# Kernel tuning notes

Measured on AMD Instinct MI355X. Metric: run time of the kernel, lower is better.

Reference implementation:

```python
import jax, jax.numpy as jnp
import numpy as np

B, T, D, H = 4096, 48, 64, 128
IMPUTE_WEIGHT = 0.3


def setup_inputs() -> dict:
    key = jax.random.key(0)
    ks = jax.random.split(key, 16)
    values = jax.random.normal(ks[0], (B, T, D), dtype=jnp.float32)
    masks = (jax.random.uniform(ks[1], (B, T, D)) < 0.7).astype(jnp.float32)
    deltas = jax.random.uniform(ks[2], (B, T, D), dtype=jnp.float32)
    s = 0.05
    return {
        "values": values, "masks": masks, "deltas": deltas,
        # TemporalDecay h (non-diag): Linear(D -> H)
        "W_td_h": jax.random.normal(ks[3], (H, D), dtype=jnp.float32) * s,
        "b_td_h": jax.random.normal(ks[4], (H,), dtype=jnp.float32) * s,
        # TemporalDecay x (diag): W is D x D but only diagonal used
        "W_td_x": jax.random.normal(ks[5], (D, D), dtype=jnp.float32) * s,
        "b_td_x": jax.random.normal(ks[6], (D,), dtype=jnp.float32) * s,
        # hist_reg: Linear(H -> D)
        "W_hist": jax.random.normal(ks[7], (D, H), dtype=jnp.float32) * s,
        "b_hist": jax.random.normal(ks[8], (D,), dtype=jnp.float32) * s,
        # feat_reg: D x D with zeroed diagonal mask
        "W_feat": jax.random.normal(ks[9], (D, D), dtype=jnp.float32) * s,
        "b_feat": jax.random.normal(ks[10], (D,), dtype=jnp.float32) * s,
        # weight_combine: Linear(2D -> D)
        "W_comb": jax.random.normal(ks[11], (D, 2 * D), dtype=jnp.float32) * s,
        "b_comb": jax.random.normal(ks[12], (D,), dtype=jnp.float32) * s,
        # LSTMCell(2D -> H), torch gate order i,f,g,o
        "W_ih": jax.random.normal(ks[13], (4 * H, 2 * D), dtype=jnp.float32) * s,
        "W_hh": jax.random.normal(ks[14], (4 * H, H), dtype=jnp.float32) * s,
        "b_ih": jnp.zeros((4 * H,), dtype=jnp.float32),
        "b_hh": jnp.zeros((4 * H,), dtype=jnp.float32),
    }


def reference(values, masks, deltas, W_td_h, b_td_h, W_td_x, b_td_x,
              W_hist, b_hist, W_feat, b_feat, W_comb, b_comb,
              W_ih, W_hh, b_ih, b_hh):
    Bn, Tn, Dn = values.shape
    Hn = W_hh.shape[1]
    w_td_x_diag = jnp.diagonal(W_td_x)                      # diag mask -> elementwise
    W_feat_m = W_feat * (1.0 - jnp.eye(Dn, dtype=W_feat.dtype))  # zero diagonal

    def step(carry, xs):
        h, c, x_loss = carry
        x, m, d = xs                                        # each [B, D]
        gamma_h = jnp.exp(-jax.nn.relu(d @ W_td_h.T + b_td_h))   # [B, H]
        gamma_x = jnp.exp(-jax.nn.relu(d * w_td_x_diag + b_td_x))  # [B, D]
        h = h * gamma_h
        x_h = h @ W_hist.T + b_hist
        denom = jnp.sum(m) + 1e-5
        x_loss = x_loss + jnp.sum(jnp.abs(x - x_h) * m) / denom
        x_c = m * x + (1.0 - m) * x_h
        z_h = x_c @ W_feat_m.T + b_feat
        x_loss = x_loss + jnp.sum(jnp.abs(x - z_h) * m) / denom
        alpha = jnp.concatenate([gamma_x, m], axis=1) @ W_comb.T + b_comb
        c_h = alpha * z_h + (1.0 - alpha) * x_h
        x_loss = x_loss + jnp.sum(jnp.abs(x - c_h) * m) / denom
        c_c = m * x + (1.0 - m) * c_h
        inp = jnp.concatenate([c_c, m], axis=1)             # [B, 2D]
        gates = inp @ W_ih.T + b_ih + h @ W_hh.T + b_hh     # [B, 4H]
        i_g, f_g, g_g, o_g = jnp.split(gates, 4, axis=1)
        c = jax.nn.sigmoid(f_g) * c + jax.nn.sigmoid(i_g) * jnp.tanh(g_g)
        h = jax.nn.sigmoid(o_g) * jnp.tanh(c)
        return (h, c, x_loss), c_c

    h0 = jnp.zeros((Bn, Hn), dtype=values.dtype)
    c0 = jnp.zeros((Bn, Hn), dtype=values.dtype)
    xs = (jnp.swapaxes(values, 0, 1), jnp.swapaxes(masks, 0, 1), jnp.swapaxes(deltas, 0, 1))
    (_, _, x_loss), imps = jax.lax.scan(step, (h0, c0, jnp.float32(0.0)), xs)
    imputations = jnp.swapaxes(imps, 0, 1)                  # [B, T, D]
    loss = x_loss * IMPUTE_WEIGHT
    return loss, imputations
```

## Files before the change

### kernel.cpp

```cpp
#include <hip/hip_runtime.h>
#include <cmath>

#define Bb 4096
#define Tt 48
#define Dd 64
#define Hh 128
#define NB 16
#define NTHR 512

#define BAR_LDS() asm volatile("s_waitcnt lgkmcnt(0)\n\ts_barrier" ::: "memory")

typedef unsigned short ushort_t;
typedef __attribute__((ext_vector_type(8))) short short8;
typedef __attribute__((ext_vector_type(4))) float floatx4;

#define WS_DEN   0
#define WS_LOSS  48
#define WS_FRAGS 64
#define FR_F 0
#define FR_A 256
#define FR_B 272
#define FR_C 288
#define FR_E 296
#define N_FRAGS 312

__device__ __forceinline__ ushort_t f2bf(float x) {
  unsigned int u = __float_as_uint(x);
  u += 0x7fffu + ((u >> 16) & 1u);
  return (ushort_t)(u >> 16);
}
__device__ __forceinline__ float sigmoidf_(float x) { return 1.0f / (1.0f + __expf(-x)); }
__device__ __forceinline__ float tanhf_(float x) { return 2.0f / (1.0f + __expf(-2.0f * x)) - 1.0f; }

__global__ void prep_kernel(const float* __restrict__ W_td_h, const float* __restrict__ W_hist,
                            const float* __restrict__ W_feat, const float* __restrict__ W_comb,
                            const float* __restrict__ W_ih, const float* __restrict__ W_hh,
                            float* __restrict__ ws) {
  int f = blockIdx.x;
  int tid = threadIdx.x;
  if (f == 0 && tid < 64) ws[tid] = 0.0f;
  ushort_t* fb = (ushort_t*)(ws + WS_FRAGS);
  #pragma unroll
  for (int u = 0; u < 2; u++) {
    int e = tid * 2 + u;
    int l = e >> 3, j = e & 7;
    int n16 = l & 15;
    int kq = ((l >> 4) << 3) + j;
    float v;
    if (f < 256) {
      int w = f >> 5, g = (f >> 3) & 3, ks = f & 7;
      int n = g * 128 + w * 16 + n16;
      int k = ks * 32 + kq;
      v = (k < 128) ? W_ih[n * 128 + k] : W_hh[n * 128 + (k - 128)];
    } else if (f < 272) {
      int ff = f - 256, w = ff >> 1, ks = ff & 1;
      int n = w * 16 + n16;
      v = W_td_h[n * 64 + ks * 32 + kq];
    } else if (f < 288) {
      int ff = f - 272, w = ff >> 2, ks = ff & 3;
      int n = w * 16 + n16;
      v = W_hist[n * 128 + ks * 32 + kq];
    } else if (f < 296) {
      int ff = f - 288, w = ff >> 1, ks = ff & 1;
      int n = w * 16 + n16;
      int k = ks * 32 + kq;
      v = (n == k) ? 0.0f : W_feat[n * 64 + k];
    } else {
      int ff = f - 296, w = ff >> 2, ks = ff & 3;
      int n = w * 16 + n16;
      v = W_comb[n * 128 + ks * 32 + kq];
    }
    fb[f * 512 + e] = f2bf(v);
  }
}

__global__ void denom_kernel(const float* __restrict__ masks, float* __restrict__ ws) {
  int t = blockIdx.x >> 4;
  int chunk = blockIdx.x & 15;
  int base = chunk * 256;
  int tid = threadIdx.x;
  int j = tid & 63;
  int brow = tid >> 6;
  float s = 0.0f;
  for (int i = 0; i < 64; i++) {
    int b = base + i * 4 + brow;
    s += masks[((size_t)b * Tt + t) * Dd + j];
  }
  for (int off = 32; off > 0; off >>= 1) s += __shfl_down(s, off, 64);
  __shared__ float red[4];
  if ((tid & 63) == 0) red[tid >> 6] = s;
  __syncthreads();
  if (tid == 0) atomicAdd(&ws[WS_DEN + t], red[0] + red[1] + red[2] + red[3]);
}

__global__ __launch_bounds__(NTHR, 2)
void main_kernel(const float* __restrict__ values, const float* __restrict__ masks,
                 const float* __restrict__ deltas, const float* __restrict__ W_td_x,
                 const float* __restrict__ b_td_h, const float* __restrict__ b_td_x,
                 const float* __restrict__ b_hist, const float* __restrict__ b_feat,
                 const float* __restrict__ b_comb,
                 const float* __restrict__ b_ih, const float* __restrict__ b_hh,
                 float* ws, float* __restrict__ out) {
  __shared__ __align__(16) ushort_t act[16 * 264];
  __shared__ __align__(16) ushort_t dbuf[16 * 72];
  __shared__ __align__(16) ushort_t gxbuf[16 * 72];
  __shared__ __align__(16) ushort_t xcbuf[16 * 72];
  __shared__ __align__(16) float xmbuf[16 * 132];
  __shared__ __align__(16) float xhbuf[16 * 68];
  __shared__ float sden[48];
  __shared__ float red[8];

  int tid = threadIdx.x;
  int w = tid >> 6;
  int lane = tid & 63;
  int l15 = lane & 15;
  int quad = lane >> 4;
  int b0 = blockIdx.x * NB;
  const ushort_t* fb = (const ushort_t*)(ws + WS_FRAGS);

  for (int i = tid; i < 48; i += NTHR) sden[i] = 1.0f / (ws[WS_DEN + i] + 1e-5f);

  short8 wF[32];
  #pragma unroll
  for (int g = 0; g < 4; g++)
    #pragma unroll
    for (int ks = 0; ks < 8; ks++)
      wF[g * 8 + ks] = *(const short8*)(fb + (size_t)(FR_F + w * 32 + g * 8 + ks) * 512 + lane * 8);
  short8 wA[2];
  #pragma unroll
  for (int ks = 0; ks < 2; ks++)
    wA[ks] = *(const short8*)(fb + (size_t)(FR_A + w * 2 + ks) * 512 + lane * 8);
  short8 wBE[4];
  short8 wC[2];
  if (w < 4) {
    #pragma unroll
    for (int ks = 0; ks < 4; ks++)
      wBE[ks] = *(const short8*)(fb + (size_t)(FR_B + w * 4 + ks) * 512 + lane * 8);
  } else {
    #pragma unroll
    for (int ks = 0; ks < 4; ks++)
      wBE[ks] = *(const short8*)(fb + (size_t)(FR_E + (w - 4) * 4 + ks) * 512 + lane * 8);
    #pragma unroll
    for (int ks = 0; ks < 2; ks++)
      wC[ks] = *(const short8*)(fb + (size_t)(FR_C + (w - 4) * 2 + ks) * 512 + lane * 8);
  }

  int colh = w * 16 + l15;
  float biasF0 = b_ih[colh]       + b_hh[colh];
  float biasF1 = b_ih[128 + colh] + b_hh[128 + colh];
  float biasF2 = b_ih[256 + colh] + b_hh[256 + colh];
  float biasF3 = b_ih[384 + colh] + b_hh[384 + colh];
  float biasA  = b_td_h[colh];
  int colD = (w & 3) * 16 + l15;
  float biasBE = (w < 4) ? b_hist[colD] : b_comb[colD];
  float biasC  = b_feat[colD];

  int e0 = tid * 2;
  int lb = e0 >> 6, li = e0 & 63;
  size_t gbase = ((size_t)(b0 + lb) * Tt) * Dd + li;
  float diag0 = W_td_x[li * 64 + li], diag1 = W_td_x[(li + 1) * 64 + (li + 1)];
  float btx0 = b_td_x[li], btx1 = b_td_x[li + 1];

  int ha[4];
  float* impp[4];
  #pragma unroll
  for (int r = 0; r < 4; r++) {
    int m = quad * 4 + r;
    ha[r] = m * 264 + 128 + colh;
    impp[r] = out + 1 + (size_t)(b0 + m) * Tt * Dd + colD;
  }

  float h_reg[4] = {0.f, 0.f, 0.f, 0.f};
  float c_reg[4] = {0.f, 0.f, 0.f, 0.f};
  float loss_acc = 0.0f;

  float2 px = *(const float2*)(values + gbase);
  float2 pm = *(const float2*)(masks + gbase);
  float2 pd = *(const float2*)(deltas + gbase);

  __syncthreads();

  for (int t = 0; t < Tt; t++) {
    BAR_LDS();
    *(float4*)(&xmbuf[lb * 132 + 2 * li]) = make_float4(px.x, pm.x, px.y, pm.y);
    *(unsigned int*)(&act[lb * 264 + 64 + li]) =
        (unsigned int)f2bf(pm.x) | ((unsigned int)f2bf(pm.y) << 16);
    *(unsigned int*)(&dbuf[lb * 72 + li]) =
        (unsigned int)f2bf(pd.x) | ((unsigned int)f2bf(pd.y) << 16);
    float g0 = __expf(-fmaxf(pd.x * diag0 + btx0, 0.0f));
    float g1 = __expf(-fmaxf(pd.y * diag1 + btx1, 0.0f));
    *(unsigned int*)(&gxbuf[lb * 72 + li]) =
        (unsigned int)f2bf(g0) | ((unsigned int)f2bf(g1) << 16);
    float invden = sden[t];
    floatx4 a0 = {biasF0, biasF0, biasF0, biasF0};
    floatx4 a1 = {biasF1, biasF1, biasF1, biasF1};
    floatx4 a2 = {biasF2, biasF2, biasF2, biasF2};
    floatx4 a3 = {biasF3, biasF3, biasF3, biasF3};
    {
      int tn = (t + 1 < Tt) ? (t + 1) : t;
      size_t g = gbase + (size_t)tn * Dd;
      px = *(const float2*)(values + g);
      pm = *(const float2*)(masks + g);
      pd = *(const float2*)(deltas + g);
    }
    BAR_LDS();

    short8 mf0 = *(const short8*)(&act[l15 * 264 + 64 + quad * 8]);
    short8 mf1 = *(const short8*)(&act[l15 * 264 + 96 + quad * 8]);
    {
      short8 df0 = *(const short8*)(&dbuf[l15 * 72 + quad * 8]);
      short8 df1 = *(const short8*)(&dbuf[l15 * 72 + 32 + quad * 8]);
      floatx4 accA = {biasA, biasA, biasA, biasA};
      accA = __builtin_amdgcn_mfma_f32_16x16x32_bf16(df0, wA[0], accA, 0, 0, 0);
      accA = __builtin_amdgcn_mfma_f32_16x16x32_bf16(df1, wA[1], accA, 0, 0, 0);
      a0 = __builtin_amdgcn_mfma_f32_16x16x32_bf16(mf0, wF[2],  a0, 0, 0, 0);
      a0 = __builtin_amdgcn_mfma_f32_16x16x32_bf16(mf1, wF[3],  a0, 0, 0, 0);
      a1 = __builtin_amdgcn_mfma_f32_16x16x32_bf16(mf0, wF[10], a1, 0, 0, 0);
      a1 = __builtin_amdgcn_mfma_f32_16x16x32_bf16(mf1, wF[11], a1, 0, 0, 0);
      a2 = __builtin_amdgcn_mfma_f32_16x16x32_bf16(mf0, wF[18], a2, 0, 0, 0);
      a2 = __builtin_amdgcn_mfma_f32_16x16x32_bf16(mf1, wF[19], a2, 0, 0, 0);
      a3 = __builtin_amdgcn_mfma_f32_16x16x32_bf16(mf0, wF[26], a3, 0, 0, 0);
      a3 = __builtin_amdgcn_mfma_f32_16x16x32_bf16(mf1, wF[27], a3, 0, 0, 0);
      #pragma unroll
      for (int r = 0; r < 4; r++) {
        h_reg[r] *= __expf(-fmaxf(accA[r], 0.0f));
        act[ha[r]] = f2bf(h_reg[r]);
      }
    }
    BAR_LDS();

    floatx4 accP = {biasBE, biasBE, biasBE, biasBE};
    {
      short8 hf0 = *(const short8*)(&act[l15 * 264 + 128 + quad * 8]);
      short8 hf1 = *(const short8*)(&act[l15 * 264 + 160 + quad * 8]);
      short8 hf2 = *(const short8*)(&act[l15 * 264 + 192 + quad * 8]);
      short8 hf3 = *(const short8*)(&act[l15 * 264 + 224 + quad * 8]);
      if (w < 4) {
        accP = __builtin_amdgcn_mfma_f32_16x16x32_bf16(hf0, wBE[0], accP, 0, 0, 0);
        accP = __builtin_amdgcn_mfma_f32_16x16x32_bf16(hf1, wBE[1], accP, 0, 0, 0);
        accP = __builtin_amdgcn_mfma_f32_16x16x32_bf16(hf2, wBE[2], accP, 0, 0, 0);
        accP = __builtin_amdgcn_mfma_f32_16x16x32_bf16(hf3, wBE[3], accP, 0, 0, 0);
      } else {
        short8 gx0 = *(const short8*)(&gxbuf[l15 * 72 + quad * 8]);
        short8 gx1 = *(const short8*)(&gxbuf[l15 * 72 + 32 + quad * 8]);
        accP = __builtin_amdgcn_mfma_f32_16x16x32_bf16(gx0, wBE[0], accP, 0, 0, 0);
        accP = __builtin_amdgcn_mfma_f32_16x16x32_bf16(gx1, wBE[1], accP, 0, 0, 0);
        accP = __builtin_amdgcn_mfma_f32_16x16x32_bf16(mf0, wBE[2], accP, 0, 0, 0);
        accP = __builtin_amdgcn_mfma_f32_16x16x32_bf16(mf1, wBE[3], accP, 0, 0, 0);
      }
      a0 = __builtin_amdgcn_mfma_f32_16x16x32_bf16(hf0, wF[4],  a0, 0, 0, 0);
      a0 = __builtin_amdgcn_mfma_f32_16x16x32_bf16(hf1, wF[5],  a0, 0, 0, 0);
      a0 = __builtin_amdgcn_mfma_f32_16x16x32_bf16(hf2, wF[6],  a0, 0, 0, 0);
      a0 = __builtin_amdgcn_mfma_f32_16x16x32_bf16(hf3, wF[7],  a0, 0, 0, 0);
      a1 = __builtin_amdgcn_mfma_f32_16x16x32_bf16(hf0, wF[12], a1, 0, 0, 0);
      a1 = __builtin_amdgcn_mfma_f32_16x16x32_bf16(hf1, wF[13], a1, 0, 0, 0);
      a1 = __builtin_amdgcn_mfma_f32_16x16x32_bf16(hf2, wF[14], a1, 0, 0, 0);
      a1 = __builtin_amdgcn_mfma_f32_16x16x32_bf16(hf3, wF[15], a1, 0, 0, 0);
      a2 = __builtin_amdgcn_mfma_f32_16x16x32_bf16(hf0, wF[20], a2, 0, 0, 0);
      a2 = __builtin_amdgcn_mfma_f32_16x16x32_bf16(hf1, wF[21], a2, 0, 0, 0);
      a2 = __builtin_amdgcn_mfma_f32_16x16x32_bf16(hf2, wF[22], a2, 0, 0, 0);
      a2 = __builtin_amdgcn_mfma_f32_16x16x32_bf16(hf3, wF[23], a2, 0, 0, 0);
      a3 = __builtin_amdgcn_mfma_f32_16x16x32_bf16(hf0, wF[28], a3, 0, 0, 0);
      a3 = __builtin_amdgcn_mfma_f32_16x16x32_bf16(hf1, wF[29], a3, 0, 0, 0);
      a3 = __builtin_amdgcn_mfma_f32_16x16x32_bf16(hf2, wF[30], a3, 0, 0, 0);
      a3 = __builtin_amdgcn_mfma_f32_16x16x32_bf16(hf3, wF[31], a3, 0, 0, 0);
      if (w < 4) {
        #pragma unroll
        for (int r = 0; r < 4; r++) {
          int m = quad * 4 + r;
          float2 xm = *(const float2*)(&xmbuf[m * 132 + 2 * colD]);
          float xh = accP[r];
          loss_acc += fabsf(xm.x - xh) * xm.y * invden;
          xhbuf[m * 68 + colD] = xh;
          xcbuf[m * 72 + colD] = f2bf(xm.y * xm.x + (1.0f - xm.y) * xh);
        }
      }
    }
    BAR_LDS();

    if (w >= 4) {
      short8 xc0 = *(const short8*)(&xcbuf[l15 * 72 + quad * 8]);
      short8 xc1 = *(const short8*)(&xcbuf[l15 * 72 + 32 + quad * 8]);
      floatx4 accC = {biasC, biasC, biasC, biasC};
      accC = __builtin_amdgcn_mfma_f32_16x16x32_bf16(xc0, wC[0], accC, 0, 0, 0);
      accC = __builtin_amdgcn_mfma_f32_16x16x32_bf16(xc1, wC[1], accC, 0, 0, 0);
      #pragma unroll
      for (int r = 0; r < 4; r++) {
        int m = quad * 4 + r;
        float2 xm = *(const float2*)(&xmbuf[m * 132 + 2 * colD]);
        float xh = xhbuf[m * 68 + colD];
        float zh = accC[r];
        float al = accP[r];
        loss_acc += fabsf(xm.x - zh) * xm.y * invden;
        float ch = al * zh + (1.0f - al) * xh;
        loss_acc += fabsf(xm.x - ch) * xm.y * invden;
        float cc = xm.y * xm.x + (1.0f - xm.y) * ch;
        *impp[r] = cc;
        impp[r] += Dd;
        act[m * 264 + colD] = f2bf(cc);
      }
    } else {
      #pragma unroll
      for (int r = 0; r < 4; r++) impp[r] += Dd;
    }
    BAR_LDS();

    {
      short8 cf0 = *(const short8*)(&act[l15 * 264 + quad * 8]);
      short8 cf1 = *(const short8*)(&act[l15 * 264 + 32 + quad * 8]);
      a0 = __builtin_amdgcn_mfma_f32_16x16x32_bf16(cf0, wF[0],  a0, 0, 0, 0);
      a0 = __builtin_amdgcn_mfma_f32_16x16x32_bf16(cf1, wF[1],  a0, 0, 0, 0);
      a1 = __builtin_amdgcn_mfma_f32_16x16x32_bf16(cf0, wF[8],  a1, 0, 0, 0);
      a1 = __builtin_amdgcn_mfma_f32_16x16x32_bf16(cf1, wF[9],  a1, 0, 0, 0);
      a2 = __builtin_amdgcn_mfma_f32_16x16x32_bf16(cf0, wF[16], a2, 0, 0, 0);
      a2 = __builtin_amdgcn_mfma_f32_16x16x32_bf16(cf1, wF[17], a2, 0, 0, 0);
      a3 = __builtin_amdgcn_mfma_f32_16x16x32_bf16(cf0, wF[24], a3, 0, 0, 0);
      a3 = __builtin_amdgcn_mfma_f32_16x16x32_bf16(cf1, wF[25], a3, 0, 0, 0);
      #pragma unroll
      for (int r = 0; r < 4; r++) {
        float ig = sigmoidf_(a0[r]);
        float fg = sigmoidf_(a1[r]);
        float gg = tanhf_(a2[r]);
        float og = sigmoidf_(a3[r]);
        c_reg[r] = fg * c_reg[r] + ig * gg;
        h_reg[r] = og * tanhf_(c_reg[r]);
      }
    }
  }

  float s = loss_acc;
  for (int off = 32; off > 0; off >>= 1) s += __shfl_down(s, off, 64);
  if (lane == 0) red[w] = s;
  __syncthreads();
  if (tid == 0) {
    float tot = 0.0f;
    #pragma unroll
    for (int i = 0; i < 8; i++) tot += red[i];
    atomicAdd(&ws[WS_LOSS], tot);
  }
}

__global__ void final_kernel(const float* __restrict__ ws, float* __restrict__ out) {
  if (threadIdx.x == 0 && blockIdx.x == 0) out[0] = 0.3f * ws[WS_LOSS];
}

extern "C" void kernel_launch(void* const* d_in, const int* in_sizes, int n_in,
                              void* d_out, int out_size, void* d_ws, size_t ws_size,
                              hipStream_t stream) {
  const float* values = (const float*)d_in[0];
  const float* masks  = (const float*)d_in[1];
  const float* deltas = (const float*)d_in[2];
  const float* W_td_h = (const float*)d_in[3];
  const float* b_td_h = (const float*)d_in[4];
  const float* W_td_x = (const float*)d_in[5];
  const float* b_td_x = (const float*)d_in[6];
  const float* W_hist = (const float*)d_in[7];
  const float* b_hist = (const float*)d_in[8];
  const float* W_feat = (const float*)d_in[9];
  const float* b_feat = (const float*)d_in[10];
  const float* W_comb = (const float*)d_in[11];
  const float* b_comb = (const float*)d_in[12];
  const float* W_ih   = (const float*)d_in[13];
  const float* W_hh   = (const float*)d_in[14];
  const float* b_ih   = (const float*)d_in[15];
  const float* b_hh   = (const float*)d_in[16];
  float* out = (float*)d_out;
  float* ws  = (float*)d_ws;

  prep_kernel<<<dim3(N_FRAGS), dim3(256), 0, stream>>>(W_td_h, W_hist, W_feat, W_comb,
                                                       W_ih, W_hh, ws);
  denom_kernel<<<dim3(48 * 16), dim3(256), 0, stream>>>(masks, ws);
  main_kernel<<<dim3(Bb / NB), dim3(NTHR), 0, stream>>>(values, masks, deltas, W_td_x,
                                                        b_td_h, b_td_x, b_hist, b_feat,
                                                        b_comb, b_ih, b_hh, ws, out);
  final_kernel<<<dim3(1), dim3(64), 0, stream>>>(ws, out);
}
```

Before: 361.8 us.

## Restructure recurrent step schedule to cut per-step barriers and pre-stage next inputs

```diff
diff --git a/kernel.cpp b/kernel.cpp
--- a/kernel.cpp
+++ b/kernel.cpp
@@ -177,42 +177,55 @@
   float2 px = *(const float2*)(values + gbase);
   float2 pm = *(const float2*)(masks + gbase);
   float2 pd = *(const float2*)(deltas + gbase);
-
-  __syncthreads();
-
-  for (int t = 0; t < Tt; t++) {
-    BAR_LDS();
-    *(float4*)(&xmbuf[lb * 132 + 2 * li]) = make_float4(px.x, pm.x, px.y, pm.y);
-    *(unsigned int*)(&act[lb * 264 + 64 + li]) =
-        (unsigned int)f2bf(pm.x) | ((unsigned int)f2bf(pm.y) << 16);
-    *(unsigned int*)(&dbuf[lb * 72 + li]) =
-        (unsigned int)f2bf(pd.x) | ((unsigned int)f2bf(pd.y) << 16);
+  #pragma unroll
+  for (int i = 0; i < 2; i++) {
+    int e = tid + i * NTHR;
+    *(unsigned int*)(&act[(e >> 6) * 264 + 128 + 2 * (e & 63)]) = 0u;
+  }
+  *(float4*)(&xmbuf[lb * 132 + 2 * li]) = make_float4(px.x, pm.x, px.y, pm.y);
+  *(unsigned int*)(&act[lb * 264 + 64 + li]) =
+      (unsigned int)f2bf(pm.x) | ((unsigned int)f2bf(pm.y) << 16);
+  {
     float g0 = __expf(-fmaxf(pd.x * diag0 + btx0, 0.0f));
     float g1 = __expf(-fmaxf(pd.y * diag1 + btx1, 0.0f));
     *(unsigned int*)(&gxbuf[lb * 72 + li]) =
         (unsigned int)f2bf(g0) | ((unsigned int)f2bf(g1) << 16);
+  }
+  {
+    size_t g = gbase + Dd;
+    px = *(const float2*)(values + g);
+    pm = *(const float2*)(masks + g);
+    pd = *(const float2*)(deltas + g);
+  }
+  __syncthreads();
+
+  for (int t = 0; t < Tt; t++) {
     float invden = sden[t];
     floatx4 a0 = {biasF0, biasF0, biasF0, biasF0};
     floatx4 a1 = {biasF1, biasF1, biasF1, biasF1};
     floatx4 a2 = {biasF2, biasF2, biasF2, biasF2};
     floatx4 a3 = {biasF3, biasF3, biasF3, biasF3};
-    {
-      int tn = (t + 1 < Tt) ? (t + 1) : t;
-      size_t g = gbase + (size_t)tn * Dd;
-      px = *(const float2*)(values + g);
-      pm = *(const float2*)(masks + g);
-      pd = *(const float2*)(deltas + g);
-    }
-    BAR_LDS();
-
-    short8 mf0 = *(const short8*)(&act[l15 * 264 + 64 + quad * 8]);
-    short8 mf1 = *(const short8*)(&act[l15 * 264 + 96 + quad * 8]);
-    {
-      short8 df0 = *(const short8*)(&dbuf[l15 * 72 + quad * 8]);
-      short8 df1 = *(const short8*)(&dbuf[l15 * 72 + 32 + quad * 8]);
-      floatx4 accA = {biasA, biasA, biasA, biasA};
-      accA = __builtin_amdgcn_mfma_f32_16x16x32_bf16(df0, wA[0], accA, 0, 0, 0);
-      accA = __builtin_amdgcn_mfma_f32_16x16x32_bf16(df1, wA[1], accA, 0, 0, 0);
+    floatx4 accP = {biasBE, biasBE, biasBE, biasBE};
+    short8 mf0, mf1;
+
+    short8 hf0 = *(const short8*)(&act[l15 * 264 + 128 + quad * 8]);
+    short8 hf1 = *(const short8*)(&act[l15 * 264 + 160 + quad * 8]);
+    short8 hf2 = *(const short8*)(&act[l15 * 264 + 192 + quad * 8]);
+    short8 hf3 = *(const short8*)(&act[l15 * 264 + 224 + quad * 8]);
+    if (w < 4) {
+      accP = __builtin_amdgcn_mfma_f32_16x16x32_bf16(hf0, wBE[0], accP, 0, 0, 0);
+      accP = __builtin_amdgcn_mfma_f32_16x16x32_bf16(hf1, wBE[1], accP, 0, 0, 0);
+      accP = __builtin_amdgcn_mfma_f32_16x16x32_bf16(hf2, wBE[2], accP, 0, 0, 0);
+      accP = __builtin_amdgcn_mfma_f32_16x16x32_bf16(hf3, wBE[3], accP, 0, 0, 0);
+    } else {
+      short8 gx0 = *(const short8*)(&gxbuf[l15 * 72 + quad * 8]);
+      short8 gx1 = *(const short8*)(&gxbuf[l15 * 72 + 32 + quad * 8]);
+      mf0 = *(const short8*)(&act[l15 * 264 + 64 + quad * 8]);
+      mf1 = *(const short8*)(&act[l15 * 264 + 96 + quad * 8]);
+      accP = __builtin_amdgcn_mfma_f32_16x16x32_bf16(gx0, wBE[0], accP, 0, 0, 0);
+      accP = __builtin_amdgcn_mfma_f32_16x16x32_bf16(gx1, wBE[1], accP, 0, 0, 0);
+      accP = __builtin_amdgcn_mfma_f32_16x16x32_bf16(mf0, wBE[2], accP, 0, 0, 0);
+      accP = __builtin_amdgcn_mfma_f32_16x16x32_bf16(mf1, wBE[3], accP, 0, 0, 0);
       a0 = __builtin_amdgcn_mfma_f32_16x16x32_bf16(mf0, wF[2],  a0, 0, 0, 0);
       a0 = __builtin_amdgcn_mfma_f32_16x16x32_bf16(mf1, wF[3],  a0, 0, 0, 0);
       a1 = __builtin_amdgcn_mfma_f32_16x16x32_bf16(mf0, wF[10], a1, 0, 0, 0);
@@ -221,69 +234,56 @@
       a2 = __builtin_amdgcn_mfma_f32_16x16x32_bf16(mf1, wF[19], a2, 0, 0, 0);
       a3 = __builtin_amdgcn_mfma_f32_16x16x32_bf16(mf0, wF[26], a3, 0, 0, 0);
       a3 = __builtin_amdgcn_mfma_f32_16x16x32_bf16(mf1, wF[27], a3, 0, 0, 0);
+    }
+    a0 = __builtin_amdgcn_mfma_f32_16x16x32_bf16(hf0, wF[4],  a0, 0, 0, 0);
+    a0 = __builtin_amdgcn_mfma_f32_16x16x32_bf16(hf1, wF[5],  a0, 0, 0, 0);
+    a0 = __builtin_amdgcn_mfma_f32_16x16x32_bf16(hf2, wF[6],  a0, 0, 0, 0);
+    a0 = __builtin_amdgcn_mfma_f32_16x16x32_bf16(hf3, wF[7],  a0, 0, 0, 0);
+    a1 = __builtin_amdgcn_mfma_f32_16x16x32_bf16(hf0, wF[12], a1, 0, 0, 0);
+    a1 = __builtin_amdgcn_mfma_f32_16x16x32_bf16(hf1, wF[13], a1, 0, 0, 0);
+    a1 = __builtin_amdgcn_mfma_f32_16x16x32_bf16(hf2, wF[14], a1, 0, 0, 0);
+    a1 = __builtin_amdgcn_mfma_f32_16x16x32_bf16(hf3, wF[15], a1, 0, 0, 0);
+    a2 = __builtin_amdgcn_mfma_f32_16x16x32_bf16(hf0, wF[20], a2, 0, 0, 0);
+    a2 = __builtin_amdgcn_mfma_f32_16x16x32_bf16(hf1, wF[21], a2, 0, 0, 0);
+    a2 = __builtin_amdgcn_mfma_f32_16x16x32_bf16(hf2, wF[22], a2, 0, 0, 0);
+    a2 = __builtin_amdgcn_mfma_f32_16x16x32_bf16(hf3, wF[23], a2, 0, 0, 0);
+    a3 = __builtin_amdgcn_mfma_f32_16x16x32_bf16(hf0, wF[28], a3, 0, 0, 0);
+    a3 = __builtin_amdgcn_mfma_f32_16x16x32_bf16(hf1, wF[29], a3, 0, 0, 0);
+    a3 = __builtin_amdgcn_mfma_f32_16x16x32_bf16(hf2, wF[30], a3, 0, 0, 0);
+    a3 = __builtin_amdgcn_mfma_f32_16x16x32_bf16(hf3, wF[31], a3, 0, 0, 0);
+    if (w < 4) {
+      float s1 = 0.0f;
       #pragma unroll
       for (int r = 0; r < 4; r++) {
-        h_reg[r] *= __expf(-fmaxf(accA[r], 0.0f));
-        act[ha[r]] = f2bf(h_reg[r]);
+        int m = quad * 4 + r;
+        float2 xm = *(const float2*)(&xmbuf[m * 132 + 2 * colD]);
+        float xh = accP[r];
+        s1 += fabsf(xm.x - xh) * xm.y;
+        xhbuf[m * 68 + colD] = xh;
+        xcbuf[m * 72 + colD] = f2bf(xm.y * xm.x + (1.0f - xm.y) * xh);
       }
+      loss_acc += s1 * invden;
     }
     BAR_LDS();
 
-    floatx4 accP = {biasBE, biasBE, biasBE, biasBE};
-    {
-      short8 hf0 = *(const short8*)(&act[l15 * 264 + 128 + quad * 8]);
-      short8 hf1 = *(const short8*)(&act[l15 * 264 + 160 + quad * 8]);
-      short8 hf2 = *(const short8*)(&act[l15 * 264 + 192 + quad * 8]);
-      short8 hf3 = *(const short8*)(&act[l15 * 264 + 224 + quad * 8]);
-      if (w < 4) {
-        accP = __builtin_amdgcn_mfma_f32_16x16x32_bf16(hf0, wBE[0], accP, 0, 0, 0);
-        accP = __builtin_amdgcn_mfma_f32_16x16x32_bf16(hf1, wBE[1], accP, 0, 0, 0);
-        accP = __builtin_amdgcn_mfma_f32_16x16x32_bf16(hf2, wBE[2], accP, 0, 0, 0);
-        accP = __builtin_amdgcn_mfma_f32_16x16x32_bf16(hf3, wBE[3], accP, 0, 0, 0);
-      } else {
-        short8 gx0 = *(const short8*)(&gxbuf[l15 * 72 + quad * 8]);
-        short8 gx1 = *(const short8*)(&gxbuf[l15 * 72 + 32 + quad * 8]);
-        accP = __builtin_amdgcn_mfma_f32_16x16x32_bf16(gx0, wBE[0], accP, 0, 0, 0);
-        accP = __builtin_amdgcn_mfma_f32_16x16x32_bf16(gx1, wBE[1], accP, 0, 0, 0);
-        accP = __builtin_amdgcn_mfma_f32_16x16x32_bf16(mf0, wBE[2], accP, 0, 0, 0);
-        accP = __builtin_amdgcn_mfma_f32_16x16x32_bf16(mf1, wBE[3], accP, 0, 0, 0);
-      }
-      a0 = __builtin_amdgcn_mfma_f32_16x16x32_bf16(hf0, wF[4],  a0, 0, 0, 0);
-      a0 = __builtin_amdgcn_mfma_f32_16x16x32_bf16(hf1, wF[5],  a0, 0, 0, 0);
-      a0 = __builtin_amdgcn_mfma_f32_16x16x32_bf16(hf2, wF[6],  a0, 0, 0, 0);
-      a0 = __builtin_amdgcn_mfma_f32_16x16x32_bf16(hf3, wF[7],  a0, 0, 0, 0);
-      a1 = __builtin_amdgcn_mfma_f32_16x16x32_bf16(hf0, wF[12], a1, 0, 0, 0);
-      a1 = __builtin_amdgcn_mfma_f32_16x16x32_bf16(hf1, wF[13], a1, 0, 0, 0);
-      a1 = __builtin_amdgcn_mfma_f32_16x16x32_bf16(hf2, wF[14], a1, 0, 0, 0);
-      a1 = __builtin_amdgcn_mfma_f32_16x16x32_bf16(hf3, wF[15], a1, 0, 0, 0);
-      a2 = __builtin_amdgcn_mfma_f32_16x16x32_bf16(hf0, wF[20], a2, 0, 0, 0);
-      a2 = __builtin_amdgcn_mfma_f32_16x16x32_bf16(hf1, wF[21], a2, 0, 0, 0);
-      a2 = __builtin_amdgcn_mfma_f32_16x16x32_bf16(hf2, wF[22], a2, 0, 0, 0);
-      a2 = __builtin_amdgcn_mfma_f32_16x16x32_bf16(hf3, wF[23], a2, 0, 0, 0);
-      a3 = __builtin_amdgcn_mfma_f32_16x16x32_bf16(hf0, wF[28], a3, 0, 0, 0);
-      a3 = __builtin_amdgcn_mfma_f32_16x16x32_bf16(hf1, wF[29], a3, 0, 0, 0);
-      a3 = __builtin_amdgcn_mfma_f32_16x16x32_bf16(hf2, wF[30], a3, 0, 0, 0);
-      a3 = __builtin_amdgcn_mfma_f32_16x16x32_bf16(hf3, wF[31], a3, 0, 0, 0);
-      if (w < 4) {
-        #pragma unroll
-        for (int r = 0; r < 4; r++) {
-          int m = quad * 4 + r;
-          float2 xm = *(const float2*)(&xmbuf[m * 132 + 2 * colD]);
-          float xh = accP[r];
-          loss_acc += fabsf(xm.x - xh) * xm.y * invden;
-          xhbuf[m * 68 + colD] = xh;
-          xcbuf[m * 72 + colD] = f2bf(xm.y * xm.x + (1.0f - xm.y) * xh);
-        }
-      }
-    }
-    BAR_LDS();
-
-    if (w >= 4) {
+    if (w < 4) {
+      mf0 = *(const short8*)(&act[l15 * 264 + 64 + quad * 8]);
+      mf1 = *(const short8*)(&act[l15 * 264 + 96 + quad * 8]);
+      a0 = __builtin_amdgcn_mfma_f32_16x16x32_bf16(mf0, wF[2],  a0, 0, 0, 0);
+      a0 = __builtin_amdgcn_mfma_f32_16x16x32_bf16(mf1, wF[3],  a0, 0, 0, 0);
+      a1 = __builtin_amdgcn_mfma_f32_16x16x32_bf16(mf0, wF[10], a1, 0, 0, 0);
+      a1 = __builtin_amdgcn_mfma_f32_16x16x32_bf16(mf1, wF[11], a1, 0, 0, 0);
+      a2 = __builtin_amdgcn_mfma_f32_16x16x32_bf16(mf0, wF[18], a2, 0, 0, 0);
+      a2 = __builtin_amdgcn_mfma_f32_16x16x32_bf16(mf1, wF[19], a2, 0, 0, 0);
+      a3 = __builtin_amdgcn_mfma_f32_16x16x32_bf16(mf0, wF[26], a3, 0, 0, 0);
+      a3 = __builtin_amdgcn_mfma_f32_16x16x32_bf16(mf1, wF[27], a3, 0, 0, 0);
+    } else {
       short8 xc0 = *(const short8*)(&xcbuf[l15 * 72 + quad * 8]);
       short8 xc1 = *(const short8*)(&xcbuf[l15 * 72 + 32 + quad * 8]);
       floatx4 accC = {biasC, biasC, biasC, biasC};
       accC = __builtin_amdgcn_mfma_f32_16x16x32_bf16(xc0, wC[0], accC, 0, 0, 0);
       accC = __builtin_amdgcn_mfma_f32_16x16x32_bf16(xc1, wC[1], accC, 0, 0, 0);
+      float s23 = 0.0f;
       #pragma unroll
       for (int r = 0; r < 4; r++) {
         int m = quad * 4 + r;
@@ -291,41 +291,63 @@
         float xh = xhbuf[m * 68 + colD];
         float zh = accC[r];
         float al = accP[r];
-        loss_acc += fabsf(xm.x - zh) * xm.y * invden;
+        s23 += fabsf(xm.x - zh) * xm.y;
         float ch = al * zh + (1.0f - al) * xh;
-        loss_acc += fabsf(xm.x - ch) * xm.y * invden;
+        s23 += fabsf(xm.x - ch) * xm.y;
         float cc = xm.y * xm.x + (1.0f - xm.y) * ch;
         *impp[r] = cc;
         impp[r] += Dd;
         act[m * 264 + colD] = f2bf(cc);
       }
-    } else {
-      #pragma unroll
-      for (int r = 0; r < 4; r++) impp[r] += Dd;
-    }
+      loss_acc += s23 * invden;
+    }
+    *(unsigned int*)(&dbuf[lb * 72 + li]) =
+        (unsigned int)f2bf(pd.x) | ((unsigned int)f2bf(pd.y) << 16);
     BAR_LDS();
 
+    short8 cf0 = *(const short8*)(&act[l15 * 264 + quad * 8]);
+    short8 cf1 = *(const short8*)(&act[l15 * 264 + 32 + quad * 8]);
+    a0 = __builtin_amdgcn_mfma_f32_16x16x32_bf16(cf0, wF[0],  a0, 0, 0, 0);
+    a0 = __builtin_amdgcn_mfma_f32_16x16x32_bf16(cf1, wF[1],  a0, 0, 0, 0);
+    a1 = __builtin_amdgcn_mfma_f32_16x16x32_bf16(cf0, wF[8],  a1, 0, 0, 0);
+    a1 = __builtin_amdgcn_mfma_f32_16x16x32_bf16(cf1, wF[9],  a1, 0, 0, 0);
+    a2 = __builtin_amdgcn_mfma_f32_16x16x32_bf16(cf0, wF[16], a2, 0, 0, 0);
+    a2 = __builtin_amdgcn_mfma_f32_16x16x32_bf16(cf1, wF[17], a2, 0, 0, 0);
+    a3 = __builtin_amdgcn_mfma_f32_16x16x32_bf16(cf0, wF[24], a3, 0, 0, 0);
+    a3 = __builtin_amdgcn_mfma_f32_16x16x32_bf16(cf1, wF[25], a3, 0, 0, 0);
+    short8 df0 = *(const short8*)(&dbuf[l15 * 72 + quad * 8]);
+    short8 df1 = *(const short8*)(&dbuf[l15 * 72 + 32 + quad * 8]);
+    floatx4 accA = {biasA, biasA, biasA, biasA};
+    accA = __builtin_amdgcn_mfma_f32_16x16x32_bf16(df0, wA[0], accA, 0, 0, 0);
+    accA = __builtin_amdgcn_mfma_f32_16x16x32_bf16(df1, wA[1], accA, 0, 0, 0);
+    #pragma unroll
+    for (int r = 0; r < 4; r++) {
+      float ig = sigmoidf_(a0[r]);
+      float fg = sigmoidf_(a1[r]);
+      float gg = tanhf_(a2[r]);
+      float og = sigmoidf_(a3[r]);
+      c_reg[r] = fg * c_reg[r] + ig * gg;
+      h_reg[r] = og * tanhf_(c_reg[r]);
+      float hd = h_reg[r] * __expf(-fmaxf(accA[r], 0.0f));
+      act[ha[r]] = f2bf(hd);
+    }
+    *(float4*)(&xmbuf[lb * 132 + 2 * li]) = make_float4(px.x, pm.x, px.y, pm.y);
+    *(unsigned int*)(&act[lb * 264 + 64 + li]) =
+        (unsigned int)f2bf(pm.x) | ((unsigned int)f2bf(pm.y) << 16);
     {
-      short8 cf0 = *(const short8*)(&act[l15 * 264 + quad * 8]);
-      short8 cf1 = *(const short8*)(&act[l15 * 264 + 32 + quad * 8]);
-      a0 = __builtin_amdgcn_mfma_f32_16x16x32_bf16(cf0, wF[0],  a0, 0, 0, 0);
-      a0 = __builtin_amdgcn_mfma_f32_16x16x32_bf16(cf1, wF[1],  a0, 0, 0, 0);
-      a1 = __builtin_amdgcn_mfma_f32_16x16x32_bf16(cf0, wF[8],  a1, 0, 0, 0);
-      a1 = __builtin_amdgcn_mfma_f32_16x16x32_bf16(cf1, wF[9],  a1, 0, 0, 0);
-      a2 = __builtin_amdgcn_mfma_f32_16x16x32_bf16(cf0, wF[16], a2, 0, 0, 0);
-      a2 = __builtin_amdgcn_mfma_f32_16x16x32_bf16(cf1, wF[17], a2, 0, 0, 0);
-      a3 = __builtin_amdgcn_mfma_f32_16x16x32_bf16(cf0, wF[24], a3, 0, 0, 0);
-      a3 = __builtin_amdgcn_mfma_f32_16x16x32_bf16(cf1, wF[25], a3, 0, 0, 0);
-      #pragma unroll
-      for (int r = 0; r < 4; r++) {
-        float ig = sigmoidf_(a0[r]);
-        float fg = sigmoidf_(a1[r]);
-        float gg = tanhf_(a2[r]);
-        float og = sigmoidf_(a3[r]);
-        c_reg[r] = fg * c_reg[r] + ig * gg;
-        h_reg[r] = og * tanhf_(c_reg[r]);
-      }
-    }
+      float g0 = __expf(-fmaxf(pd.x * diag0 + btx0, 0.0f));
+      float g1 = __expf(-fmaxf(pd.y * diag1 + btx1, 0.0f));
+      *(unsigned int*)(&gxbuf[lb * 72 + li]) =
+          (unsigned int)f2bf(g0) | ((unsigned int)f2bf(g1) << 16);
+    }
+    {
+      int tn = (t + 2 < Tt) ? (t + 2) : (Tt - 1);
+      size_t g = gbase + (size_t)tn * Dd;
+      px = *(const float2*)(values + g);
+      pm = *(const float2*)(masks + g);
+      pd = *(const float2*)(deltas + g);
+    }
+    BAR_LDS();
   }
 
   float s = loss_acc;
```

New measurement: 357.5 us. Within noise of the previous version (-1.2%).
